# Optimization experiments

Hardware: AMD Instinct MI355X
Metric: run time of the kernel (lower is better)

The kernel has to match this reference:

```python
import jax, jax.numpy as jnp
import numpy as np

N = 8192
F_IN = 512
F_OUT = 256
NEG_SLOPE = 0.01  # F.leaky_relu default
MASK_VAL = -1000000000000000.0


def setup_inputs() -> dict:
    key = jax.random.key(0)
    k1, k2, k3, k4 = jax.random.split(key, 4)
    stdv = 1.0 / np.sqrt(F_OUT)
    x = jax.random.normal(k1, (N, F_IN), dtype=jnp.float32)
    weight = jax.random.uniform(k2, (F_IN, F_OUT), dtype=jnp.float32, minval=-stdv, maxval=stdv)
    att_vec = jax.random.normal(k3, (2 * F_OUT, 1), dtype=jnp.float32) * 0.05
    adj = jax.random.randint(k4, (N, N), 0, 2, dtype=jnp.int32)
    return {"x": x, "weight": weight, "att_vec": att_vec, "adj": adj}


def _pair_indices(n):
    # Reproduces the (buggy-but-faithful) torch.cat(dim=0).view(n,-1,2f) indexing:
    # element (i,j,:f)  = out[idx(2m)], element (i,j,f:) = out[idx(2m+1)], m = i*n+j
    # idx(r) = r // n if r < n*n else (r - n*n) % n
    nn_ = n * n
    m = jnp.arange(nn_, dtype=jnp.int32)
    r0 = 2 * m
    r1 = r0 + 1
    idx1 = jnp.where(r0 < nn_, r0 // n, (r0 - nn_) % n)
    idx2 = jnp.where(r1 < nn_, r1 // n, (r1 - nn_) % n)
    return idx1, idx2


def reference(x, weight, att_vec, adj):
    n = x.shape[0]
    f = weight.shape[1]
    # dropout p=0.0 -> identity
    out = x @ weight                      # (n, f)
    a1 = att_vec[:f, 0]                   # (f,)
    a2 = att_vec[f:, 0]                   # (f,)
    s1 = out @ a1                         # (n,)
    s2 = out @ a2                         # (n,)
    idx1, idx2 = _pair_indices(n)
    scores = (s1[idx1] + s2[idx2]).reshape(n, n)
    scores = jax.nn.leaky_relu(scores, NEG_SLOPE)
    scores = jnp.where(adj > 0, scores, MASK_VAL)
    attn = jax.nn.softmax(scores, axis=1)  # F.softmax default dim=1 for 2D
    return jax.nn.sigmoid(attn @ out)      # (n, f)
```

## Files before the change

kernel.cpp:

```cpp
#include <hip/hip_runtime.h>

using u32 = unsigned int;
using u16 = unsigned short;

typedef __attribute__((ext_vector_type(8)))  __bf16 bf16x8;
typedef __attribute__((ext_vector_type(16))) float  f32x16;
typedef __attribute__((ext_vector_type(4)))  float  f32x4;
typedef __attribute__((ext_vector_type(4)))  int    i32x4;

__device__ __forceinline__ u32 f2bf(float f){
  u32 u = __float_as_uint(f);
  return (u + 0x7FFFu + ((u >> 16) & 1u)) >> 16;
}
__device__ __forceinline__ u32 pack2bf(float lo, float hi){
  return f2bf(lo) | (f2bf(hi) << 16);
}
__device__ __forceinline__ float bfu2f(u32 us){ return __uint_as_float(us << 16); }
__device__ __forceinline__ float lrelu(float x){ return x > 0.f ? x : 0.01f * x; }

__global__ void k0_wt(const float* __restrict__ w, u16* __restrict__ wT){
  int u = blockIdx.x * 256 + threadIdx.x;
  int k = u >> 8, n = u & 255;
  wT[(size_t)n * 512 + k] = (u16)f2bf(w[(size_t)k * 256 + n]);
}

__global__ __launch_bounds__(512, 2) void k1_gemm(const float* __restrict__ x,
    const u16* __restrict__ wT, const float* __restrict__ av, u16* __restrict__ outF,
    float* __restrict__ v0, float* __restrict__ v1, u16* __restrict__ pbf){
  __shared__ float tb[8][32][36];
  __shared__ float afl[512];
  __shared__ float sred[2][32][17];
  __shared__ float srw[2][32];
  const int i0 = blockIdx.x * 32;
  const int tid = threadIdx.x;
  const int lane = tid & 63, wv = tid >> 6;
  const int r = lane & 31, h = lane >> 5;
  const float* xp = x + (size_t)(i0 + r) * 512 + h * 8;
  const u16*   bp = wT + (size_t)(wv * 32 + r) * 512 + h * 8;
  f32x16 acc = {};
  for (int s = 0; s < 32; ++s){
    f32x4 a0 = *(const f32x4*)xp;
    f32x4 a1 = *(const f32x4*)(xp + 4);
    i32x4 pk = { (int)pack2bf(a0[0], a0[1]), (int)pack2bf(a0[2], a0[3]),
                 (int)pack2bf(a1[0], a1[1]), (int)pack2bf(a1[2], a1[3]) };
    bf16x8 af = __builtin_bit_cast(bf16x8, pk);
    bf16x8 bf = *(const bf16x8*)bp;
    acc = __builtin_amdgcn_mfma_f32_32x32x16_bf16(af, bf, acc, 0, 0, 0);
    xp += 16; bp += 16;
  }
  #pragma unroll
  for (int re = 0; re < 16; ++re){
    int rr = (re & 3) + 8 * (re >> 2) + 4 * h;
    tb[wv][r][rr] = acc[re];
  }
  afl[tid] = av[tid];
  __syncthreads();
  {
    const int n2 = lane >> 1, ic = (lane & 1) * 16;
    const float* tp = &tb[wv][n2][ic];
    i32x4 w0 = { (int)pack2bf(tp[0],tp[1]),   (int)pack2bf(tp[2],tp[3]),
                 (int)pack2bf(tp[4],tp[5]),   (int)pack2bf(tp[6],tp[7]) };
    i32x4 w1 = { (int)pack2bf(tp[8],tp[9]),   (int)pack2bf(tp[10],tp[11]),
                 (int)pack2bf(tp[12],tp[13]), (int)pack2bf(tp[14],tp[15]) };
    const int n = wv * 32 + n2;
    const int k16 = (i0 + ic) >> 4;
    u16* op = outF + ((size_t)k16 * 256 + n) * 16;
    *(i32x4*)op = w0;
    *((i32x4*)op + 1) = w1;
  }
  const int row = tid & 31, g = tid >> 5;
  const int w8 = g >> 1, fh = (g & 1) * 16;
  float a1c = 0.f, a2c = 0.f;
  #pragma unroll
  for (int f = 0; f < 16; ++f){
    float tv = tb[w8][fh + f][row];
    a1c = fmaf(tv, afl[w8 * 32 + fh + f], a1c);
    a2c = fmaf(tv, afl[256 + w8 * 32 + fh + f], a2c);
  }
  sred[0][row][g] = a1c; sred[1][row][g] = a2c;
  __syncthreads();
  if (tid < 64){
    int which = tid >> 5, r2 = tid & 31;
    float s = 0.f;
    #pragma unroll
    for (int g2 = 0; g2 < 16; ++g2) s += sred[which][r2][g2];
    srw[which][r2] = s;
  }
  __syncthreads();
  if (tid < 16){
    int k = (i0 >> 1) + tid;
    float sa  = srw[0][2*tid],   sb  = srw[1][2*tid];
    float sa1 = srw[0][2*tid+1], sb1 = srw[1][2*tid+1];
    v0[k] = lrelu(sa + sb);
    v1[k] = lrelu(sa1 + sb1);
    float w = lrelu(sa + sb1);
    pbf[k] = (u16)f2bf(__expf(w));
  }
}

__global__ __launch_bounds__(512, 2) void k3_main(const int* __restrict__ adj,
    const u16* __restrict__ outF, const u16* __restrict__ pbf,
    float* __restrict__ P, float* __restrict__ pd){
  __shared__ u16 Ab[2][4096];
  __shared__ u32 pl32[1024];
  __shared__ float dred[32][66];
  const int bid = blockIdx.x;
  const int xcd = bid & 7, slot = bid >> 3;
  const int c = xcd >> 1;
  const int tile = (xcd & 1) * 128 + slot;
  const bool top = tile < 128;
  const int i0 = tile * 32;
  const int kbase = c * 2048;
  const int pb = tile * 4 + c;
  const int tid = threadIdx.x, l = tid & 63, w = tid >> 6;
  const int r = l & 31, h = l >> 5;
  const int fb = w * 32;
  const int* aq0 = adj + (size_t)(i0 + w) * 8192 + kbase + l * 4;
  const u16* bq0 = outF + ((size_t)(kbase >> 4) * 256 + fb + r) * 16 + h * 8;

  if (top){
    pl32[tid] = 0x3F803F80u; pl32[tid + 512] = 0x3F803F80u;
  } else {
    const u32* ps = (const u32*)pbf + (c & 1) * 1024;
    pl32[tid] = ps[tid]; pl32[tid + 512] = ps[tid + 512];
  }
  __syncthreads();

  i32x4 ar[4];
  bf16x8 BA[8], BB[8];
  f32x16 acc = {};
  float d4[4] = {0.f, 0.f, 0.f, 0.f};

#define ADJ_ISS(PP_) { \
  _Pragma("unroll") for (int q = 0; q < 4; ++q) \
    ar[q] = *(const i32x4*)(aq0 + (size_t)q * 65536 + (PP_) * 256); \
  asm volatile("" ::: "memory"); }

#define B_ISS(B_,T_) { const u16* bb_ = bq0 + (size_t)(T_) * 32768; \
  _Pragma("unroll") for (int j = 0; j < 8; ++j) \
    B_[j] = *(const bf16x8*)(bb_ + j * 4096); \
  asm volatile("" ::: "memory"); }

#define MFMA8(B_,BUF_) { const u16* rb_ = &Ab[BUF_][0] + r * 16 + h * 8; \
  __builtin_amdgcn_s_setprio(1); \
  _Pragma("unroll") for (int j = 0; j < 8; ++j){ \
    bf16x8 a_ = *(const bf16x8*)(rb_ + j * 512); \
    acc = __builtin_amdgcn_mfma_f32_32x32x16_bf16(a_, B_[j], acc, 0, 0, 0); } \
  __builtin_amdgcn_s_setprio(0); }

#define PACKW(H_,BUF_,PP_) { \
  if ((l >> 5) == (H_)){ \
    const int ks_ = (l & 31) >> 2; \
    u32 pv0_ = pl32[(PP_) * 128 + l * 2]; \
    u32 pv1_ = pl32[(PP_) * 128 + l * 2 + 1]; \
    u16* wb_ = &Ab[BUF_][0] + ks_ * 512 + (l & 3) * 4; \
    _Pragma("unroll") for (int q = 0; q < 4; ++q){ \
      i32x4 a_ = ar[q]; \
      u32 w0_ = ((((u32)(-a_[0])) & 0xFFFFu) | (((u32)(-a_[1])) << 16)) & pv0_; \
      u32 w1_ = ((((u32)(-a_[2])) & 0xFFFFu) | (((u32)(-a_[3])) << 16)) & pv1_; \
      d4[q] += __uint_as_float(w0_ << 16) + __uint_as_float(w0_ & 0xFFFF0000u) \
             + __uint_as_float(w1_ << 16) + __uint_as_float(w1_ & 0xFFFF0000u); \
      uint2 wv_; wv_.x = w0_; wv_.y = w1_; \
      *(uint2*)(wb_ + (q * 8 + w) * 16) = wv_; } } }

#define KBAR() { asm volatile("s_waitcnt lgkmcnt(0)" ::: "memory"); \
  __builtin_amdgcn_s_barrier(); asm volatile("" ::: "memory"); }

  ADJ_ISS(0);
  B_ISS(BA, 0);
  PACKW(0, 0, 0);
  KBAR();
  #pragma unroll 1
  for (int pp = 0; pp < 8; ++pp){
    const int e = 2 * pp;
    B_ISS(BB, e + 1);
    MFMA8(BA, 0);
    PACKW(1, 1, pp);
    if (pp < 7) ADJ_ISS(pp + 1);
    KBAR();
    if (pp < 7){
      B_ISS(BA, e + 2);
      MFMA8(BB, 1);
      PACKW(0, 0, pp + 1);
      KBAR();
    }
  }
  MFMA8(BB, 1);

#undef ADJ_ISS
#undef B_ISS
#undef MFMA8
#undef PACKW
#undef KBAR

  #pragma unroll
  for (int q = 0; q < 4; ++q) dred[q * 8 + w][l] = d4[q];
  __syncthreads();
  if (tid < 32){
    float s = 0.f;
    #pragma unroll
    for (int j = 0; j < 64; ++j) s += dred[tid][j];
    pd[(size_t)pb * 32 + tid] = s;
  }
  float* Pb = P + (size_t)pb * 8192 + fb + r;
  #pragma unroll
  for (int e2 = 0; e2 < 16; ++e2){
    int rr = (e2 & 3) + 8 * (e2 >> 2) + 4 * h;
    __builtin_nontemporal_store(acc[e2], Pb + (size_t)rr * 256);
  }
}

__global__ void k4_final(const float* __restrict__ P, const float* __restrict__ pd,
    const float* __restrict__ v0, const float* __restrict__ v1, float* __restrict__ out){
  const int i = blockIdx.x, n = threadIdx.x;
  const int tile = i >> 5, rloc = i & 31;
  const size_t base = (size_t)tile * 32768 + (size_t)rloc * 256 + n;
  float P0 = __builtin_nontemporal_load(P + base);
  float P1 = __builtin_nontemporal_load(P + base + 8192);
  float P2 = __builtin_nontemporal_load(P + base + 16384);
  float P3 = __builtin_nontemporal_load(P + base + 24576);
  const float* pdp = pd + (size_t)tile * 128 + rloc;
  float d0 = pdp[0], d1 = pdp[32], d2 = pdp[64], d3 = pdp[96];
  float val;
  if (i < 4096){
    float va = v0[i], vb = v1[i];
    float m = fmaxf(va, vb);
    float e0 = __expf(va - m), e1 = __expf(vb - m);
    val = (e0 * (P0 + P1) + e1 * (P2 + P3)) / (e0 * (d0 + d1) + e1 * (d2 + d3));
  } else {
    val = (P0 + P1 + P2 + P3) / (d0 + d1 + d2 + d3);
  }
  out[(size_t)i * 256 + n] = 1.0f / (1.0f + __expf(-val));
}

extern "C" void kernel_launch(void* const* d_in, const int* in_sizes, int n_in,
                              void* d_out, int out_size, void* d_ws, size_t ws_size,
                              hipStream_t stream)
{
  const float* x      = (const float*)d_in[0];
  const float* weight = (const float*)d_in[1];
  const float* av     = (const float*)d_in[2];
  const int*   adj    = (const int*)d_in[3];
  float* out = (float*)d_out;
  char* ws = (char*)d_ws;
  float* P     = (float*)(ws + 0);
  float* pd    = (float*)(ws + 33554432);
  u16*   outF  = (u16*)  (ws + 33685504);
  u16*   wT    = (u16*)  (ws + 37879808);
  u16*   pbf   = (u16*)  (ws + 38141952);
  float* v0    = (float*)(ws + 38150144);
  float* v1    = (float*)(ws + 38166528);

  k0_wt    <<<512, 256, 0, stream>>>(weight, wT);
  k1_gemm  <<<256, 512, 0, stream>>>(x, wT, av, outF, v0, v1, pbf);
  k3_main  <<<1024, 512, 0, stream>>>(adj, outF, pbf, P, pd);
  k4_final <<<8192, 256, 0, stream>>>(P, pd, v0, v1, out);
}
```

Baseline: 116.8 us.

## Halve k-split in main attention GEMM with deeper pipelined LDS tiles

The main adj·out kernel now splits the 8192-long reduction into 2 chunks instead of 4, so it launches 512 blocks that each handle 4096 columns. Each stage stages a larger 512-column adjacency tile in padded LDS, and global B loads are issued in smaller groups of four interleaved with the MFMAs. The row-sum reduction now uses wavefront shuffles instead of an LDS table, and the final kernel combines 2 partials instead of 4. This halves the partial-sum traffic and the XCD/tile mapping changes. The cost is more LDS per block and fewer blocks, which may reduce occupancy and parallelism.

```diff
diff --git a/kernel.cpp b/kernel.cpp
--- a/kernel.cpp
+++ b/kernel.cpp
@@ -101,112 +101,119 @@
 __global__ __launch_bounds__(512, 2) void k3_main(const int* __restrict__ adj,
     const u16* __restrict__ outF, const u16* __restrict__ pbf,
     float* __restrict__ P, float* __restrict__ pd){
-  __shared__ u16 Ab[2][4096];
-  __shared__ u32 pl32[1024];
-  __shared__ float dred[32][66];
+  __shared__ u16 AbS[2][16896];
+  __shared__ u32 plS[2048];
+  __shared__ float dshS[32];
   const int bid = blockIdx.x;
   const int xcd = bid & 7, slot = bid >> 3;
-  const int c = xcd >> 1;
-  const int tile = (xcd & 1) * 128 + slot;
+  const int c = xcd & 1;
+  const int tile = (xcd >> 1) * 64 + slot;
   const bool top = tile < 128;
   const int i0 = tile * 32;
-  const int kbase = c * 2048;
-  const int pb = tile * 4 + c;
+  const int pb = tile * 2 + c;
   const int tid = threadIdx.x, l = tid & 63, w = tid >> 6;
   const int r = l & 31, h = l >> 5;
   const int fb = w * 32;
-  const int* aq0 = adj + (size_t)(i0 + w) * 8192 + kbase + l * 4;
-  const u16* bq0 = outF + ((size_t)(kbase >> 4) * 256 + fb + r) * 16 + h * 8;
+  const int* aq0 = adj + (size_t)(i0 + w) * 8192 + c * 4096 + l * 4;
+  const u16* bq0 = outF + (size_t)c * 1048576 + (fb + r) * 16 + h * 8;
 
   if (top){
-    pl32[tid] = 0x3F803F80u; pl32[tid + 512] = 0x3F803F80u;
+    plS[tid] = 0x3F803F80u; plS[tid + 512] = 0x3F803F80u;
+    plS[tid + 1024] = 0x3F803F80u; plS[tid + 1536] = 0x3F803F80u;
   } else {
-    const u32* ps = (const u32*)pbf + (c & 1) * 1024;
-    pl32[tid] = ps[tid]; pl32[tid + 512] = ps[tid + 512];
-  }
-  __syncthreads();
-
-  i32x4 ar[4];
-  bf16x8 BA[8], BB[8];
+    const u32* ps = (const u32*)pbf;
+    plS[tid] = ps[tid]; plS[tid + 512] = ps[tid + 512];
+    plS[tid + 1024] = ps[tid + 1024]; plS[tid + 1536] = ps[tid + 1536];
+  }
+  __syncthreads();
+
+  i32x4 ar[8];
+  bf16x8 BA[4], BB[4];
   f32x16 acc = {};
   float d4[4] = {0.f, 0.f, 0.f, 0.f};
 
-#define ADJ_ISS(PP_) { \
-  _Pragma("unroll") for (int q = 0; q < 4; ++q) \
-    ar[q] = *(const i32x4*)(aq0 + (size_t)q * 65536 + (PP_) * 256); \
+#define ADJ_H(HF_,PH_) { \
+  _Pragma("unroll") for (int j_ = 0; j_ < 2; ++j_){ \
+    const int q_ = (HF_) * 2 + j_; \
+    const int* ap_ = aq0 + q_ * 65536 + (PH_) * 512; \
+    ar[q_*2]   = *(const i32x4*)ap_; \
+    ar[q_*2+1] = *(const i32x4*)(ap_ + 256); } \
   asm volatile("" ::: "memory"); }
 
-#define B_ISS(B_,T_) { const u16* bb_ = bq0 + (size_t)(T_) * 32768; \
-  _Pragma("unroll") for (int j = 0; j < 8; ++j) \
-    B_[j] = *(const bf16x8*)(bb_ + j * 4096); \
+#define B_ISS4(B_,G_) { const u16* bb_ = bq0 + (size_t)(G_) * 4096; \
+  B_[0] = *(const bf16x8*)bb_;            B_[1] = *(const bf16x8*)(bb_ + 4096); \
+  B_[2] = *(const bf16x8*)(bb_ + 8192);   B_[3] = *(const bf16x8*)(bb_ + 12288); \
   asm volatile("" ::: "memory"); }
 
-#define MFMA8(B_,BUF_) { const u16* rb_ = &Ab[BUF_][0] + r * 16 + h * 8; \
+#define MFMA4(B_,RB_,S_) { \
   __builtin_amdgcn_s_setprio(1); \
-  _Pragma("unroll") for (int j = 0; j < 8; ++j){ \
-    bf16x8 a_ = *(const bf16x8*)(rb_ + j * 512); \
-    acc = __builtin_amdgcn_mfma_f32_32x32x16_bf16(a_, B_[j], acc, 0, 0, 0); } \
+  _Pragma("unroll") for (int j_ = 0; j_ < 4; ++j_){ \
+    bf16x8 a_ = *(const bf16x8*)((RB_) + ((S_) * 4 + j_) * 528 + r * 16 + h * 8); \
+    acc = __builtin_amdgcn_mfma_f32_32x32x16_bf16(a_, B_[j_], acc, 0, 0, 0); } \
   __builtin_amdgcn_s_setprio(0); }
 
-#define PACKW(H_,BUF_,PP_) { \
-  if ((l >> 5) == (H_)){ \
-    const int ks_ = (l & 31) >> 2; \
-    u32 pv0_ = pl32[(PP_) * 128 + l * 2]; \
-    u32 pv1_ = pl32[(PP_) * 128 + l * 2 + 1]; \
-    u16* wb_ = &Ab[BUF_][0] + ks_ * 512 + (l & 3) * 4; \
-    _Pragma("unroll") for (int q = 0; q < 4; ++q){ \
-      i32x4 a_ = ar[q]; \
-      u32 w0_ = ((((u32)(-a_[0])) & 0xFFFFu) | (((u32)(-a_[1])) << 16)) & pv0_; \
-      u32 w1_ = ((((u32)(-a_[2])) & 0xFFFFu) | (((u32)(-a_[3])) << 16)) & pv1_; \
-      d4[q] += __uint_as_float(w0_ << 16) + __uint_as_float(w0_ & 0xFFFF0000u) \
-             + __uint_as_float(w1_ << 16) + __uint_as_float(w1_ & 0xFFFF0000u); \
+#define PACK(PH_,WB_) { \
+  _Pragma("unroll") for (int q_ = 0; q_ < 4; ++q_){ \
+    const int row_ = q_ * 8 + w; \
+    _Pragma("unroll") for (int L_ = 0; L_ < 2; ++L_){ \
+      i32x4 a_ = ar[q_*2 + L_]; \
+      uint2 pp_ = *(const uint2*)(plS + (((PH_) & 7) * 256 + L_ * 128 + 2 * l)); \
+      u32 w0_ = ((((u32)(-a_[0])) & 0xFFFFu) | (((u32)(-a_[1])) << 16)) & pp_.x; \
+      u32 w1_ = ((((u32)(-a_[2])) & 0xFFFFu) | (((u32)(-a_[3])) << 16)) & pp_.y; \
+      d4[q_] += __uint_as_float(w0_ << 16) + __uint_as_float(w0_ & 0xFFFF0000u) \
+              + __uint_as_float(w1_ << 16) + __uint_as_float(w1_ & 0xFFFF0000u); \
+      const int slot_ = L_ * 16 + (l >> 2); \
       uint2 wv_; wv_.x = w0_; wv_.y = w1_; \
-      *(uint2*)(wb_ + (q * 8 + w) * 16) = wv_; } } }
+      *(uint2*)((WB_) + slot_ * 528 + row_ * 16 + (l & 3) * 4) = wv_; } } }
 
 #define KBAR() { asm volatile("s_waitcnt lgkmcnt(0)" ::: "memory"); \
   __builtin_amdgcn_s_barrier(); asm volatile("" ::: "memory"); }
 
-  ADJ_ISS(0);
-  B_ISS(BA, 0);
-  PACKW(0, 0, 0);
+  ADJ_H(0, 0); ADJ_H(1, 0);
+  B_ISS4(BA, 0);
+  PACK(0, &AbS[0][0]);
   KBAR();
+
   #pragma unroll 1
-  for (int pp = 0; pp < 8; ++pp){
-    const int e = 2 * pp;
-    B_ISS(BB, e + 1);
-    MFMA8(BA, 0);
-    PACKW(1, 1, pp);
-    if (pp < 7) ADJ_ISS(pp + 1);
-    KBAR();
-    if (pp < 7){
-      B_ISS(BA, e + 2);
-      MFMA8(BB, 1);
-      PACKW(0, 0, pp + 1);
+  for (int t = 0; t < 8; ++t){
+    const u16* rb = &AbS[t & 1][0];
+    u16* wb = &AbS[(t + 1) & 1][0];
+    #pragma unroll
+    for (int s = 0; s < 8; ++s){
+      if (!(t == 7 && s == 7)){
+        const int g = t * 32 + (s + 1) * 4;
+        if (s & 1){ B_ISS4(BA, g); } else { B_ISS4(BB, g); }
+      }
+      if (t < 7 && s == 0) ADJ_H(0, t + 1);
+      if (t < 7 && s == 1) ADJ_H(1, t + 1);
+      if (s & 1){ MFMA4(BB, rb, s); } else { MFMA4(BA, rb, s); }
+    }
+    if (t < 7){
+      PACK(t + 1, wb);
       KBAR();
     }
   }
-  MFMA8(BB, 1);
-
-#undef ADJ_ISS
-#undef B_ISS
-#undef MFMA8
-#undef PACKW
+
+#undef ADJ_H
+#undef B_ISS4
+#undef MFMA4
+#undef PACK
 #undef KBAR
 
   #pragma unroll
-  for (int q = 0; q < 4; ++q) dred[q * 8 + w][l] = d4[q];
-  __syncthreads();
-  if (tid < 32){
-    float s = 0.f;
+  for (int q = 0; q < 4; ++q){
+    float v = d4[q];
     #pragma unroll
-    for (int j = 0; j < 64; ++j) s += dred[tid][j];
-    pd[(size_t)pb * 32 + tid] = s;
-  }
+    for (int mk = 1; mk < 64; mk <<= 1) v += __shfl_xor(v, mk);
+    if (l == 0) dshS[q * 8 + w] = v;
+  }
+  __syncthreads();
+  if (tid < 32) pd[(size_t)pb * 32 + tid] = dshS[tid];
   float* Pb = P + (size_t)pb * 8192 + fb + r;
   #pragma unroll
-  for (int e2 = 0; e2 < 16; ++e2){
-    int rr = (e2 & 3) + 8 * (e2 >> 2) + 4 * h;
-    __builtin_nontemporal_store(acc[e2], Pb + (size_t)rr * 256);
+  for (int e = 0; e < 16; ++e){
+    int rr = (e & 3) + 8 * (e >> 2) + 4 * h;
+    __builtin_nontemporal_store(acc[e], Pb + (size_t)rr * 256);
   }
 }
 
@@ -214,21 +221,19 @@
     const float* __restrict__ v0, const float* __restrict__ v1, float* __restrict__ out){
   const int i = blockIdx.x, n = threadIdx.x;
   const int tile = i >> 5, rloc = i & 31;
-  const size_t base = (size_t)tile * 32768 + (size_t)rloc * 256 + n;
+  const size_t base = (size_t)tile * 16384 + (size_t)rloc * 256 + n;
   float P0 = __builtin_nontemporal_load(P + base);
   float P1 = __builtin_nontemporal_load(P + base + 8192);
-  float P2 = __builtin_nontemporal_load(P + base + 16384);
-  float P3 = __builtin_nontemporal_load(P + base + 24576);
-  const float* pdp = pd + (size_t)tile * 128 + rloc;
-  float d0 = pdp[0], d1 = pdp[32], d2 = pdp[64], d3 = pdp[96];
+  float d0 = pd[tile * 64 + rloc];
+  float d1 = pd[tile * 64 + 32 + rloc];
   float val;
   if (i < 4096){
     float va = v0[i], vb = v1[i];
     float m = fmaxf(va, vb);
     float e0 = __expf(va - m), e1 = __expf(vb - m);
-    val = (e0 * (P0 + P1) + e1 * (P2 + P3)) / (e0 * (d0 + d1) + e1 * (d2 + d3));
+    val = (e0 * P0 + e1 * P1) / (e0 * d0 + e1 * d1);
   } else {
-    val = (P0 + P1 + P2 + P3) / (d0 + d1 + d2 + d3);
+    val = (P0 + P1) / (d0 + d1);
   }
   out[(size_t)i * 256 + n] = 1.0f / (1.0f + __expf(-val));
 }
@@ -244,15 +249,15 @@
   float* out = (float*)d_out;
   char* ws = (char*)d_ws;
   float* P     = (float*)(ws + 0);
-  float* pd    = (float*)(ws + 33554432);
-  u16*   outF  = (u16*)  (ws + 33685504);
-  u16*   wT    = (u16*)  (ws + 37879808);
-  u16*   pbf   = (u16*)  (ws + 38141952);
-  float* v0    = (float*)(ws + 38150144);
-  float* v1    = (float*)(ws + 38166528);
+  float* pd    = (float*)(ws + 16777216);
+  u16*   outF  = (u16*)  (ws + 16842752);
+  u16*   wT    = (u16*)  (ws + 21037056);
+  u16*   pbf   = (u16*)  (ws + 21299200);
+  float* v0    = (float*)(ws + 21307392);
+  float* v1    = (float*)(ws + 21323776);
 
   k0_wt    <<<512, 256, 0, stream>>>(weight, wT);
   k1_gemm  <<<256, 512, 0, stream>>>(x, wT, av, outF, v0, v1, pbf);
-  k3_main  <<<1024, 512, 0, stream>>>(adj, outF, pbf, P, pd);
+  k3_main  <<<512, 512, 0, stream>>>(adj, outF, pbf, P, pd);
   k4_final <<<8192, 256, 0, stream>>>(P, pd, v0, v1, out);
 }
```

Result: no change. 115.6 us (-1.1%).
